# Kernel optimization log

Hardware: AMD Instinct MI355X
Metric: run time of the kernel (lower is better)

## Reference

```python
import jax, jax.numpy as jnp
import numpy as np

# ---- config (from init_kwargs) ----
XBOUND = (-51.2, 51.2, 0.8)
YBOUND = (-51.2, 51.2, 0.8)
ZBOUND = (-3.0, 1.0, 0.5)
FINAL_DIM = (512, 512)   # (H, W) of raw images
XV, YV, ZV = 128, 128, 8  # voxel grid dims from bounds
EPS = 1e-6


def setup_inputs() -> dict:
    key = jax.random.key(0)
    kf, ki, ke = jax.random.split(key, 3)
    feats = jax.random.normal(kf, (2, 4, 64, 64, 64), jnp.float32)   # B,N,C,Hf,Wf (post-CamEncode)
    intrins = jax.random.normal(ki, (2, 4, 4, 4), jnp.float32)       # B,N,4,4 pix_T_cam
    extrins = jax.random.normal(ke, (2, 4, 4, 4), jnp.float32)       # B,N,4,4 cam0_T_camX
    return {"feats": feats, "intrins": intrins, "extrins": extrins}


def _safe_inverse(a):
    # rigid-transform inverse: R^T, -R^T t; last row copied through (geom.safe_inverse)
    rT = jnp.swapaxes(a[:, :3, :3], 1, 2)
    t = -jnp.einsum('bij,bj->bi', rT, a[:, :3, 3])
    top = jnp.concatenate([rT, t[:, :, None]], axis=2)
    return jnp.concatenate([top, a[:, 3:4, :]], axis=1)


def _scale_intrinsics(K, sx, sy):
    # geom.scale_intrinsics: rebuild clean 4x4 intrinsics with scaled fx,fy,x0,y0
    BN = K.shape[0]
    Kn = jnp.zeros((BN, 4, 4), K.dtype)
    Kn = Kn.at[:, 0, 0].set(K[:, 0, 0] * sx)
    Kn = Kn.at[:, 1, 1].set(K[:, 1, 1] * sy)
    Kn = Kn.at[:, 0, 2].set(K[:, 0, 2] * sx)
    Kn = Kn.at[:, 1, 2].set(K[:, 1, 2] * sy)
    Kn = Kn.at[:, 2, 2].set(1.0)
    Kn = Kn.at[:, 3, 3].set(1.0)
    return Kn


def _grid_sample_zeros(feat, x, y):
    # F.grid_sample(..., align_corners=False, padding='zeros') at pixel coords (x,y)
    # feat: (BN,C,H,W); x,y: (BN,P)
    BN, C, H, W = feat.shape
    px = x - 0.5  # unnormalized sample position (align_corners=False)
    py = y - 0.5
    x0f = jnp.floor(px); y0f = jnp.floor(py)
    wx = px - x0f; wy = py - y0f
    x0 = x0f.astype(jnp.int32); y0 = y0f.astype(jnp.int32)
    featf = feat.reshape(BN, C, H * W)

    def corner(xi, yi, w):
        valid = (xi >= 0) & (xi < W) & (yi >= 0) & (yi < H)
        idx = jnp.clip(yi, 0, H - 1) * W + jnp.clip(xi, 0, W - 1)
        g = jnp.take_along_axis(featf, idx[:, None, :], axis=2)  # (BN,C,P)
        return g * (w * valid.astype(w.dtype))[:, None, :]

    return (corner(x0, y0, (1 - wx) * (1 - wy)) + corner(x0 + 1, y0, wx * (1 - wy))
            + corner(x0, y0 + 1, (1 - wx) * wy) + corner(x0 + 1, y0 + 1, wx * wy))


def _mem_grid_cam0():
    # gridcloud3d (Z,Y,X order) mapped Mem->Ref: ref = mem*vox + MIN + vox/2
    vsx = (XBOUND[1] - XBOUND[0]) / XV
    vsy = (YBOUND[1] - YBOUND[0]) / YV
    vsz = (ZBOUND[1] - ZBOUND[0]) / ZV
    gz, gy, gx = jnp.meshgrid(jnp.arange(ZV, dtype=jnp.float32),
                              jnp.arange(YV, dtype=jnp.float32),
                              jnp.arange(XV, dtype=jnp.float32), indexing='ij')
    xc = gx * vsx + (XBOUND[0] + vsx / 2)
    yc = gy * vsy + (YBOUND[0] + vsy / 2)
    zc = gz * vsz + (ZBOUND[0] + vsz / 2)
    return jnp.stack([xc, yc, zc], axis=-1).reshape(ZV * YV * XV, 3)  # (P,3)


def reference(feats, intrins, extrins):
    B, N, C, Hf, Wf = feats.shape
    BN = B * N
    feats_ = feats.reshape(BN, C, Hf, Wf)
    K = intrins.reshape(BN, 4, 4)
    E = extrins.reshape(BN, 4, 4)

    camX_T_cam0 = _safe_inverse(E)
    sy = Hf / float(FINAL_DIM[0])
    sx = Wf / float(FINAL_DIM[1])
    featpix_T_cam = _scale_intrinsics(K, sx, sy)
    pix_T_cam0 = jnp.einsum('bij,bjk->bik', featpix_T_cam, camX_T_cam0)

    xyz_cam0 = _mem_grid_cam0()  # (P,3)

    def apply44(T, p):  # (BN,4,4) x (P,3) -> (BN,P,3)
        return jnp.einsum('bij,pj->bpi', T[:, :3, :3], p) + T[:, None, :3, 3]

    xyz_camX = apply44(camX_T_cam0, xyz_cam0)
    z = xyz_camX[..., 2]
    xyz_pix = apply44(pix_T_cam0, xyz_cam0)
    denom = jnp.maximum(xyz_pix[..., 2:3], EPS)  # clamp(min=EPS)
    x = xyz_pix[..., 0] / denom[..., 0]
    y = xyz_pix[..., 1] / denom[..., 0]

    valid = ((x > -0.5) & (x < float(Wf) - 0.5) & (y > -0.5) & (y < float(Hf) - 0.5)
             & (z > 0.0)).astype(feats.dtype)  # (BN,P)

    vals = _grid_sample_zeros(feats_, x, y) * valid[:, None, :]  # (BN,C,P)
    feat_mems = vals.reshape(B, N, C, ZV, YV, XV)

    mask = (jnp.abs(feat_mems) > 0).astype(feats.dtype)
    feat_mem = jnp.sum(feat_mems * mask, axis=1) / (EPS + jnp.sum(mask, axis=1))  # (B,C,Z,Y,X)

    feat_mem = jnp.transpose(feat_mem, (0, 1, 4, 3, 2))      # b c X Y Z (permute 0,1,4,3,2)
    out = jnp.transpose(feat_mem, (0, 1, 4, 2, 3)).reshape(B, C * ZV, XV, YV)  # b (c z) h w
    return out
```

## Files before the change

### kernel.cpp

```cpp
#include <hip/hip_runtime.h>

#define BB     2
#define NN     4
#define CC     64
#define HF     64
#define WF     64
#define XVOX   128
#define YVOX   128
#define ZVOX   8
#define BN_TOT (BB * NN)
#define FEATS_PER_BN (CC * HF * WF)
#define OUT_C_STRIDE (ZVOX * XVOX * YVOX)
#define OUT_B_STRIDE (CC * OUT_C_STRIDE)

__global__ void prep_mats_kernel(const float* __restrict__ intrins,
                                 const float* __restrict__ extrins,
                                 float* __restrict__ mats) {
    int bn = threadIdx.x;
    if (bn >= BN_TOT) return;
    const float* e = extrins + bn * 16;
    const float* k = intrins + bn * 16;

    float inv[3][4];
#pragma unroll
    for (int i = 0; i < 3; ++i) {
        inv[i][0] = e[0 * 4 + i];
        inv[i][1] = e[1 * 4 + i];
        inv[i][2] = e[2 * 4 + i];
        inv[i][3] = -(e[0 * 4 + i] * e[0 * 4 + 3] +
                      e[1 * 4 + i] * e[1 * 4 + 3] +
                      e[2 * 4 + i] * e[2 * 4 + 3]);
    }
    float fx = k[0] * 0.125f;
    float fy = k[5] * 0.125f;
    float cx = k[2] * 0.125f;
    float cy = k[6] * 0.125f;

    float* m = mats + bn * 12;
#pragma unroll
    for (int j = 0; j < 4; ++j) {
        m[j]     = fx * inv[0][j] + cx * inv[2][j];
        m[4 + j] = fy * inv[1][j] + cy * inv[2][j];
        m[8 + j] = inv[2][j];
    }
}

__global__ __launch_bounds__(256) void transpose_feats_kernel(
    const float* __restrict__ in, float* __restrict__ outT) {
    __shared__ float tile[64 * 65];
    int bh = blockIdx.x;
    int bn = bh >> 6;
    int h  = bh & 63;
    int t  = threadIdx.x;

    const float* src = in + bn * FEATS_PER_BN + h * WF;
#pragma unroll
    for (int k = 0; k < 16; ++k) {
        int idx = t + k * 256;
        int c = idx >> 6;
        int w = idx & 63;
        tile[w * 65 + c] = src[c * (HF * WF) + w];
    }
    __syncthreads();
    float* dst = outT + bn * FEATS_PER_BN + h * (WF * CC);
#pragma unroll
    for (int k = 0; k < 16; ++k) {
        int idx = t + k * 256;
        int w = idx >> 6;
        int c = idx & 63;
        dst[w * CC + c] = tile[w * 65 + c];
    }
}

__global__ __launch_bounds__(256) void bev_splat_kernel(
    const float* __restrict__ featsT,
    const float* __restrict__ mats,
    float* __restrict__ out) {
    int tid = blockIdx.x * 256 + threadIdx.x;
    int vy = tid & 127;
    int vx = (tid >> 7) & 127;
    int vz = (tid >> 14) & 7;
    int b  = tid >> 17;

    float xc = vx * 0.8f - 50.8f;
    float yc = vy * 0.8f - 50.8f;
    float zc = vz * 0.5f - 2.75f;

    int   offs[4][4];
    float wgt[4][4];
    bool  act[4];

#pragma unroll
    for (int n = 0; n < NN; ++n) {
        int bn = b * NN + n;
        const float* M = mats + bn * 12;
        float px = M[0] * xc + M[1] * yc + M[2]  * zc + M[3];
        float py = M[4] * xc + M[5] * yc + M[6]  * zc + M[7];
        float pz = M[8] * xc + M[9] * yc + M[10] * zc + M[11];
        float denom = fmaxf(pz, 1e-6f);
        float sx = px / denom;
        float sy = py / denom;
        bool valid = (sx > -0.5f) && (sx < (float)WF - 0.5f) &&
                     (sy > -0.5f) && (sy < (float)HF - 0.5f) && (pz > 0.0f);
        act[n] = valid;
        int base = bn * FEATS_PER_BN;
        if (valid) {
            float gx = sx - 0.5f;
            float gy = sy - 0.5f;
            float x0f = floorf(gx), y0f = floorf(gy);
            float wx = gx - x0f,    wy = gy - y0f;
            int x0 = (int)x0f, y0 = (int)y0f;
            int xs[2]  = {x0, x0 + 1};
            int ys[2]  = {y0, y0 + 1};
            float wxs[2] = {1.0f - wx, wx};
            float wys[2] = {1.0f - wy, wy};
#pragma unroll
            for (int ky = 0; ky < 2; ++ky) {
#pragma unroll
                for (int kx = 0; kx < 2; ++kx) {
                    int kk = ky * 2 + kx;
                    int xi = xs[kx], yi = ys[ky];
                    bool cv = (xi >= 0) && (xi < WF) && (yi >= 0) && (yi < HF);
                    int xic = min(max(xi, 0), WF - 1);
                    int yic = min(max(yi, 0), HF - 1);
                    offs[n][kk] = base + (yic * WF + xic) * CC;
                    wgt[n][kk]  = cv ? (wxs[kx] * wys[ky]) : 0.0f;
                }
            }
        } else {
#pragma unroll
            for (int kk = 0; kk < 4; ++kk) { offs[n][kk] = base; wgt[n][kk] = 0.0f; }
        }
    }

    int out_base = b * OUT_B_STRIDE + vz * (XVOX * YVOX) + vx * YVOX + vy;

    if (!(act[0] || act[1] || act[2] || act[3])) {
#pragma unroll
        for (int c = 0; c < CC; ++c) out[out_base + c * OUT_C_STRIDE] = 0.0f;
        return;
    }

#pragma unroll 4
    for (int c4 = 0; c4 < CC / 4; ++c4) {
        float num0 = 0.f, num1 = 0.f, num2 = 0.f, num3 = 0.f;
        float cnt0 = 0.f, cnt1 = 0.f, cnt2 = 0.f, cnt3 = 0.f;
#pragma unroll
        for (int n = 0; n < NN; ++n) {
            if (!act[n]) continue;
            float v0 = 0.f, v1 = 0.f, v2 = 0.f, v3 = 0.f;
#pragma unroll
            for (int kk = 0; kk < 4; ++kk) {
                const float4 g =
                    *reinterpret_cast<const float4*>(featsT + offs[n][kk] + c4 * 4);
                float w = wgt[n][kk];
                v0 += w * g.x; v1 += w * g.y; v2 += w * g.z; v3 += w * g.w;
            }
            num0 += v0; num1 += v1; num2 += v2; num3 += v3;
            cnt0 += (v0 != 0.0f) ? 1.0f : 0.0f;
            cnt1 += (v1 != 0.0f) ? 1.0f : 0.0f;
            cnt2 += (v2 != 0.0f) ? 1.0f : 0.0f;
            cnt3 += (v3 != 0.0f) ? 1.0f : 0.0f;
        }
        int c0 = c4 * 4;
        out[out_base + (c0 + 0) * OUT_C_STRIDE] = num0 / (1e-6f + cnt0);
        out[out_base + (c0 + 1) * OUT_C_STRIDE] = num1 / (1e-6f + cnt1);
        out[out_base + (c0 + 2) * OUT_C_STRIDE] = num2 / (1e-6f + cnt2);
        out[out_base + (c0 + 3) * OUT_C_STRIDE] = num3 / (1e-6f + cnt3);
    }
}

extern "C" void kernel_launch(void* const* d_in, const int* in_sizes, int n_in,
                              void* d_out, int out_size, void* d_ws, size_t ws_size,
                              hipStream_t stream) {
    const float* feats   = (const float*)d_in[0];
    const float* intrins = (const float*)d_in[1];
    const float* extrins = (const float*)d_in[2];
    float* out = (float*)d_out;

    float* featsT = (float*)d_ws;
    float* mats   = featsT + BN_TOT * FEATS_PER_BN;

    prep_mats_kernel<<<1, 64, 0, stream>>>(intrins, extrins, mats);
    transpose_feats_kernel<<<BN_TOT * HF, 256, 0, stream>>>(feats, featsT);

    int total = BB * ZVOX * XVOX * YVOX;
    bev_splat_kernel<<<total / 256, 256, 0, stream>>>(featsT, mats, out);
}
```

Before: 109.6 us.

## Map channels to lanes and stage outputs in shared memory for coalesced writes

```diff
diff --git a/kernel.cpp b/kernel.cpp
--- a/kernel.cpp
+++ b/kernel.cpp
@@ -12,38 +12,6 @@
 #define FEATS_PER_BN (CC * HF * WF)
 #define OUT_C_STRIDE (ZVOX * XVOX * YVOX)
 #define OUT_B_STRIDE (CC * OUT_C_STRIDE)
-
-__global__ void prep_mats_kernel(const float* __restrict__ intrins,
-                                 const float* __restrict__ extrins,
-                                 float* __restrict__ mats) {
-    int bn = threadIdx.x;
-    if (bn >= BN_TOT) return;
-    const float* e = extrins + bn * 16;
-    const float* k = intrins + bn * 16;
-
-    float inv[3][4];
-#pragma unroll
-    for (int i = 0; i < 3; ++i) {
-        inv[i][0] = e[0 * 4 + i];
-        inv[i][1] = e[1 * 4 + i];
-        inv[i][2] = e[2 * 4 + i];
-        inv[i][3] = -(e[0 * 4 + i] * e[0 * 4 + 3] +
-                      e[1 * 4 + i] * e[1 * 4 + 3] +
-                      e[2 * 4 + i] * e[2 * 4 + 3]);
-    }
-    float fx = k[0] * 0.125f;
-    float fy = k[5] * 0.125f;
-    float cx = k[2] * 0.125f;
-    float cy = k[6] * 0.125f;
-
-    float* m = mats + bn * 12;
-#pragma unroll
-    for (int j = 0; j < 4; ++j) {
-        m[j]     = fx * inv[0][j] + cx * inv[2][j];
-        m[4 + j] = fy * inv[1][j] + cy * inv[2][j];
-        m[8 + j] = inv[2][j];
-    }
-}
 
 __global__ __launch_bounds__(256) void transpose_feats_kernel(
     const float* __restrict__ in, float* __restrict__ outT) {
@@ -74,99 +42,112 @@
 
 __global__ __launch_bounds__(256) void bev_splat_kernel(
     const float* __restrict__ featsT,
-    const float* __restrict__ mats,
+    const float* __restrict__ intrins,
+    const float* __restrict__ extrins,
     float* __restrict__ out) {
-    int tid = blockIdx.x * 256 + threadIdx.x;
-    int vy = tid & 127;
-    int vx = (tid >> 7) & 127;
-    int vz = (tid >> 14) & 7;
-    int b  = tid >> 17;
+    __shared__ float tile[64 * 65];
+    __shared__ float mats_s[NN * 12];
+
+    int blk  = blockIdx.x;
+    int half = blk & 1;
+    int vx   = (blk >> 1) & 127;
+    int vz   = (blk >> 8) & 7;
+    int b    = blk >> 11;
+
+    if (threadIdx.x < NN) {
+        int n  = threadIdx.x;
+        int bn = b * NN + n;
+        const float* e = extrins + bn * 16;
+        const float* k = intrins + bn * 16;
+        float inv[3][4];
+#pragma unroll
+        for (int i = 0; i < 3; ++i) {
+            inv[i][0] = e[0 * 4 + i];
+            inv[i][1] = e[1 * 4 + i];
+            inv[i][2] = e[2 * 4 + i];
+            inv[i][3] = -(e[0 * 4 + i] * e[0 * 4 + 3] +
+                          e[1 * 4 + i] * e[1 * 4 + 3] +
+                          e[2 * 4 + i] * e[2 * 4 + 3]);
+        }
+        float fx = k[0] * 0.125f;
+        float fy = k[5] * 0.125f;
+        float cx = k[2] * 0.125f;
+        float cy = k[6] * 0.125f;
+        float* m = mats_s + n * 12;
+#pragma unroll
+        for (int j = 0; j < 4; ++j) {
+            m[j]     = fx * inv[0][j] + cx * inv[2][j];
+            m[4 + j] = fy * inv[1][j] + cy * inv[2][j];
+            m[8 + j] = inv[2][j];
+        }
+    }
+    __syncthreads();
+
+    int wave = threadIdx.x >> 6;
+    int lane = threadIdx.x & 63;
+    int vy0  = half * 64;
 
     float xc = vx * 0.8f - 50.8f;
-    float yc = vy * 0.8f - 50.8f;
     float zc = vz * 0.5f - 2.75f;
 
-    int   offs[4][4];
-    float wgt[4][4];
-    bool  act[4];
+    for (int i = 0; i < 16; ++i) {
+        int v  = wave * 16 + i;
+        int vy = vy0 + v;
+        float yc = vy * 0.8f - 50.8f;
 
+        float num = 0.0f;
+        float cnt = 0.0f;
 #pragma unroll
-    for (int n = 0; n < NN; ++n) {
-        int bn = b * NN + n;
-        const float* M = mats + bn * 12;
-        float px = M[0] * xc + M[1] * yc + M[2]  * zc + M[3];
-        float py = M[4] * xc + M[5] * yc + M[6]  * zc + M[7];
-        float pz = M[8] * xc + M[9] * yc + M[10] * zc + M[11];
-        float denom = fmaxf(pz, 1e-6f);
-        float sx = px / denom;
-        float sy = py / denom;
-        bool valid = (sx > -0.5f) && (sx < (float)WF - 0.5f) &&
-                     (sy > -0.5f) && (sy < (float)HF - 0.5f) && (pz > 0.0f);
-        act[n] = valid;
-        int base = bn * FEATS_PER_BN;
-        if (valid) {
+        for (int n = 0; n < NN; ++n) {
+            const float* M = mats_s + n * 12;
+            float px = M[0] * xc + M[1] * yc + M[2]  * zc + M[3];
+            float py = M[4] * xc + M[5] * yc + M[6]  * zc + M[7];
+            float pz = M[8] * xc + M[9] * yc + M[10] * zc + M[11];
+            float denom = fmaxf(pz, 1e-6f);
+            float sx = px / denom;
+            float sy = py / denom;
+            bool valid = (sx > -0.5f) && (sx < (float)WF - 0.5f) &&
+                         (sy > -0.5f) && (sy < (float)HF - 0.5f) && (pz > 0.0f);
+            if (!valid) continue;
+
             float gx = sx - 0.5f;
             float gy = sy - 0.5f;
             float x0f = floorf(gx), y0f = floorf(gy);
             float wx = gx - x0f,    wy = gy - y0f;
             int x0 = (int)x0f, y0 = (int)y0f;
-            int xs[2]  = {x0, x0 + 1};
-            int ys[2]  = {y0, y0 + 1};
+            int   xs[2]  = {x0, x0 + 1};
+            int   ys[2]  = {y0, y0 + 1};
             float wxs[2] = {1.0f - wx, wx};
             float wys[2] = {1.0f - wy, wy};
+            const float* fb = featsT + (b * NN + n) * FEATS_PER_BN;
+
+            float val = 0.0f;
 #pragma unroll
             for (int ky = 0; ky < 2; ++ky) {
 #pragma unroll
                 for (int kx = 0; kx < 2; ++kx) {
-                    int kk = ky * 2 + kx;
                     int xi = xs[kx], yi = ys[ky];
                     bool cv = (xi >= 0) && (xi < WF) && (yi >= 0) && (yi < HF);
-                    int xic = min(max(xi, 0), WF - 1);
-                    int yic = min(max(yi, 0), HF - 1);
-                    offs[n][kk] = base + (yic * WF + xic) * CC;
-                    wgt[n][kk]  = cv ? (wxs[kx] * wys[ky]) : 0.0f;
+                    float w = cv ? (wxs[kx] * wys[ky]) : 0.0f;
+                    if (w != 0.0f) {
+                        val += w * fb[(yi * WF + xi) * CC + lane];
+                    }
                 }
             }
-        } else {
+            num += val;
+            cnt += (val != 0.0f) ? 1.0f : 0.0f;
+        }
+        tile[v * 65 + lane] = num / (1e-6f + cnt);
+    }
+    __syncthreads();
+
+    int base = b * OUT_B_STRIDE + vz * (XVOX * YVOX) + vx * YVOX + vy0;
 #pragma unroll
-            for (int kk = 0; kk < 4; ++kk) { offs[n][kk] = base; wgt[n][kk] = 0.0f; }
-        }
-    }
-
-    int out_base = b * OUT_B_STRIDE + vz * (XVOX * YVOX) + vx * YVOX + vy;
-
-    if (!(act[0] || act[1] || act[2] || act[3])) {
-#pragma unroll
-        for (int c = 0; c < CC; ++c) out[out_base + c * OUT_C_STRIDE] = 0.0f;
-        return;
-    }
-
-#pragma unroll 4
-    for (int c4 = 0; c4 < CC / 4; ++c4) {
-        float num0 = 0.f, num1 = 0.f, num2 = 0.f, num3 = 0.f;
-        float cnt0 = 0.f, cnt1 = 0.f, cnt2 = 0.f, cnt3 = 0.f;
-#pragma unroll
-        for (int n = 0; n < NN; ++n) {
-            if (!act[n]) continue;
-            float v0 = 0.f, v1 = 0.f, v2 = 0.f, v3 = 0.f;
-#pragma unroll
-            for (int kk = 0; kk < 4; ++kk) {
-                const float4 g =
-                    *reinterpret_cast<const float4*>(featsT + offs[n][kk] + c4 * 4);
-                float w = wgt[n][kk];
-                v0 += w * g.x; v1 += w * g.y; v2 += w * g.z; v3 += w * g.w;
-            }
-            num0 += v0; num1 += v1; num2 += v2; num3 += v3;
-            cnt0 += (v0 != 0.0f) ? 1.0f : 0.0f;
-            cnt1 += (v1 != 0.0f) ? 1.0f : 0.0f;
-            cnt2 += (v2 != 0.0f) ? 1.0f : 0.0f;
-            cnt3 += (v3 != 0.0f) ? 1.0f : 0.0f;
-        }
-        int c0 = c4 * 4;
-        out[out_base + (c0 + 0) * OUT_C_STRIDE] = num0 / (1e-6f + cnt0);
-        out[out_base + (c0 + 1) * OUT_C_STRIDE] = num1 / (1e-6f + cnt1);
-        out[out_base + (c0 + 2) * OUT_C_STRIDE] = num2 / (1e-6f + cnt2);
-        out[out_base + (c0 + 3) * OUT_C_STRIDE] = num3 / (1e-6f + cnt3);
+    for (int it = 0; it < 16; ++it) {
+        int idx = threadIdx.x + it * 256;
+        int c = idx >> 6;
+        int v = idx & 63;
+        out[base + c * OUT_C_STRIDE + v] = tile[v * 65 + c];
     }
 }
 
@@ -179,11 +160,9 @@
     float* out = (float*)d_out;
 
     float* featsT = (float*)d_ws;
-    float* mats   = featsT + BN_TOT * FEATS_PER_BN;
 
-    prep_mats_kernel<<<1, 64, 0, stream>>>(intrins, extrins, mats);
     transpose_feats_kernel<<<BN_TOT * HF, 256, 0, stream>>>(feats, featsT);
 
-    int total = BB * ZVOX * XVOX * YVOX;
-    bev_splat_kernel<<<total / 256, 256, 0, stream>>>(featsT, mats, out);
+    int nblk = BB * ZVOX * XVOX * 2;
+    bev_splat_kernel<<<nblk, 256, 0, stream>>>(featsT, intrins, extrins, out);
 }
```

Result: slower. 174.9 us (+59.5%).
